# Performance work log

Measured on AMD Instinct MI355X. Metric: run time of the kernel, lower is better.

## Reference

```python
import jax, jax.numpy as jnp
import numpy as np

N_NODES = 100000
IN_CH = 128
HID = 128
OUT_CH = 40
K = 3
N_EDGES = 3200000


def setup_inputs() -> dict:
    key = jax.random.key(0)
    ks = jax.random.split(key, 10)
    x = jax.random.normal(ks[0], (N_NODES, IN_CH), dtype=jnp.float32)
    edge_index = jax.random.randint(ks[1], (2, N_EDGES), 0, N_NODES, dtype=jnp.int64)
    s1 = 1.0 / np.sqrt(IN_CH)
    lin1_w = jax.random.uniform(ks[2], (IN_CH, HID), minval=-s1, maxval=s1, dtype=jnp.float32)
    lin1_b = jax.random.uniform(ks[3], (HID,), minval=-s1, maxval=s1, dtype=jnp.float32)
    s2 = 1.0 / np.sqrt(HID)
    gcn_w = jax.random.uniform(ks[4], (K, HID, HID), minval=-s2, maxval=s2, dtype=jnp.float32)
    gcn_b = jnp.zeros((K, HID), dtype=jnp.float32)
    lin2_w = jax.random.uniform(ks[5], (HID, OUT_CH), minval=-s2, maxval=s2, dtype=jnp.float32)
    lin2_b = jax.random.uniform(ks[6], (OUT_CH,), minval=-s2, maxval=s2, dtype=jnp.float32)
    return {"x": x, "edge_index": edge_index, "lin1_w": lin1_w, "lin1_b": lin1_b,
            "gcn_w": gcn_w, "gcn_b": gcn_b, "lin2_w": lin2_w, "lin2_b": lin2_b}


def _gcn_conv(h, w, b, src, dst, norm, n):
    # PyG GCNConv: transform, then symmetric-normalized aggregation (self-loops
    # already included in src/dst/norm), then bias.
    h = h @ w  # [N, H]
    msg = h[src] * norm[:, None]  # [E+N, H] gathered edge messages
    out = jax.ops.segment_sum(msg, dst, num_segments=n)
    return out + b


def reference(x, edge_index, lin1_w, lin1_b, gcn_w, gcn_b, lin2_w, lin2_b):
    n = x.shape[0]
    src, dst = edge_index[0], edge_index[1]
    # add self-loops (GCNConv default add_self_loops=True)
    loop = jnp.arange(n, dtype=src.dtype)
    src = jnp.concatenate([src, loop])
    dst = jnp.concatenate([dst, loop])
    # symmetric normalization D^{-1/2} (A+I) D^{-1/2}
    deg = jax.ops.segment_sum(jnp.ones(src.shape[0], dtype=x.dtype), dst, num_segments=n)
    dinv = jnp.where(deg > 0, jax.lax.rsqrt(deg), 0.0)
    norm = dinv[src] * dinv[dst]  # [E+N]

    h = jax.nn.relu(x @ lin1_w + lin1_b)  # dropout: eval mode (identity)
    for k in range(K):
        h = jax.nn.relu(_gcn_conv(h, gcn_w[k], gcn_b[k], src, dst, norm, n))
    logits = h @ lin2_w + lin2_b
    return jax.nn.log_softmax(logits, axis=1)
```

## Files before the change

kernel.cpp:

```cpp
#include <hip/hip_runtime.h>
#include <math.h>

#define NN 100000
#define NP 100032
#define HIDC 128
#define OUTC 40
#define NBUCK ((NN + 511) >> 9)
#define PT_TILE 2048
#define BCAP 18368

typedef __attribute__((ext_vector_type(2))) float floatx2;
typedef __attribute__((ext_vector_type(4))) float floatx4;
typedef __attribute__((ext_vector_type(8))) short short8;

__device__ __forceinline__ unsigned pack_bf16x2(float a, float b) {
  unsigned ua = __float_as_uint(a), ub = __float_as_uint(b);
  ua = ua + 0x7fff + ((ua >> 16) & 1);
  ub = ub + 0x7fff + ((ub >> 16) & 1);
  return (ua >> 16) | (ub & 0xffff0000u);
}
__device__ __forceinline__ unsigned short bf16r(float x) {
  unsigned u = __float_as_uint(x);
  u = u + 0x7fff + ((u >> 16) & 1);
  return (unsigned short)(u >> 16);
}


__global__ __launch_bounds__(256) void partition_kernel(
    const int* __restrict__ src, const int* __restrict__ dst,
    int* __restrict__ bcur, unsigned* __restrict__ pairs, int E) {
  __shared__ int hist[256];
  __shared__ int base[256];
  __shared__ int lcur[256];
  int t = threadIdx.x;
  hist[t] = 0; lcur[t] = 0;
  __syncthreads();
  int e0 = blockIdx.x * PT_TILE;
  int ec = E - e0; if (ec > PT_TILE) ec = PT_TILE;
  for (int i = t; i < ec; i += 256)
    atomicAdd(&hist[dst[e0 + i] >> 9], 1);
  __syncthreads();
  if (hist[t] > 0) base[t] = atomicAdd(&bcur[t], hist[t]);
  __syncthreads();
  for (int i = t; i < ec; i += 256) {
    int d = dst[e0 + i], s = src[e0 + i];
    int b = d >> 9;
    int pos = atomicAdd(&lcur[b], 1);
    pairs[base[b] + pos] = ((unsigned)(d & 511) << 17) | (unsigned)s;
  }
}

__global__ __launch_bounds__(1024) void bucket_fill_kernel(
    const unsigned* __restrict__ pairs, const int* __restrict__ bcur,
    float* __restrict__ dinv, int* __restrict__ csr,
    int* __restrict__ sbeg, int* __restrict__ send,
    float* __restrict__ sdinv, int* __restrict__ sdn, int N) {
  int b = blockIdx.x;
  int d0 = b << 9;
  int nd = N - d0; if (nd > 512) nd = 512;
  __shared__ int hist[512];
  __shared__ int cur[512];
  __shared__ int sums[512];
  int t = threadIdx.x;
  if (t < 512) hist[t] = 0;
  __syncthreads();
  int rbeg = b * BCAP, rend = bcur[b];
  for (int i = rbeg + t; i < rend; i += 1024)
    atomicAdd(&hist[pairs[i] >> 17], 1);
  __syncthreads();
  int h = 0;
  if (t < 512) { h = hist[t]; sums[t] = h; }
  __syncthreads();
  for (int off = 1; off < 512; off <<= 1) {
    int u = (t < 512 && t >= off) ? sums[t - off] : 0;
    __syncthreads();
    if (t < 512) sums[t] += u;
    __syncthreads();
  }
  int base = 0; float di = 0.f;
  if (t < 512) {
    base = rbeg + sums[t] - h;
    di = rsqrtf((float)(h + 1));
    if (t < nd) { dinv[d0 + t] = di; cur[t] = base; }
  }
  __syncthreads();

  if (t < 128) hist[t] = 0;
  __syncthreads();
  int c = h < 127 ? h : 127;
  if (t < nd) atomicAdd(&hist[c], 1);
  __syncthreads();
  int dv = (t < 128) ? hist[t] : 0;
  if (t < 128) sums[t] = dv;
  __syncthreads();
  for (int off = 1; off < 128; off <<= 1) {
    int u = (t < 128 && t >= off) ? sums[t - off] : 0;
    __syncthreads();
    if (t < 128) sums[t] += u;
    __syncthreads();
  }
  if (t < 128) hist[128 + t] = sums[t] - dv;
  __syncthreads();
  if (t < nd) {
    int pos = d0 + atomicAdd(&hist[128 + c], 1);
    sbeg[pos] = base; send[pos] = base + h; sdinv[pos] = di; sdn[pos] = d0 + t;
  }
  __syncthreads();

  for (int i = rbeg + t; i < rend; i += 1024) {
    unsigned pk = pairs[i];
    int q = atomicAdd(&cur[pk >> 17], 1);
    csr[q] = pk & 0x1FFFF;
  }
}


__global__ __launch_bounds__(256) void prep_misc_kernel(
    const float* __restrict__ lin1_w, const float* __restrict__ gcn_w,
    const float* __restrict__ lin2_w, int* __restrict__ bcur,
    unsigned short* __restrict__ Wt, unsigned short* __restrict__ W2t) {
  int b = blockIdx.x;
  int t = threadIdx.x;
  if (b == 0) {
    if (t < NBUCK) bcur[t] = t * BCAP;
  } else if (b <= 32) {
    int m = (b - 1) >> 3;
    int chunk = (b - 1) & 7;
    const float* src = (m == 0) ? lin1_w : (gcn_w + (size_t)(m - 1) * 16384);
    unsigned short* dstp = Wt + (size_t)m * 16384;
    int i0 = chunk * 2048;
    for (int i = i0 + t; i < i0 + 2048; i += 256) {
      int n = i >> 7, k = i & 127;
      dstp[(size_t)n * 128 + k] = bf16r(src[(size_t)k * 128 + n]);
    }
  } else {
    int chunk = b - 33;
    int i0 = chunk * 3072;
    for (int i = i0 + t; i < i0 + 3072; i += 256) {
      int n = i >> 7, k = i & 127;
      W2t[i] = (n < OUTC) ? bf16r(lin2_w[(size_t)k * OUTC + n]) : (unsigned short)0;
    }
  }
}


template <int MODE>
__global__ __launch_bounds__(256) void gemm_mfma_kernel(
    const void* __restrict__ Av, const unsigned short* __restrict__ Wt,
    const float* __restrict__ bias, const float* __restrict__ dinv,
    void* __restrict__ Y, int M) {
  int t = threadIdx.x;
  int w = t >> 6;
  int l = t & 63;
  int quad = l >> 4;
  int m16 = l & 15;
  int row0 = blockIdx.x * 64;
  int colbase = w * 32;

  floatx4 acc[4][2];
#pragma unroll
  for (int rt = 0; rt < 4; rt++)
#pragma unroll
    for (int ct = 0; ct < 2; ct++) acc[rt][ct] = (floatx4)0.f;

#pragma unroll
  for (int kc = 0; kc < 4; kc++) {
    int kof = kc * 32 + quad * 8;
    short8 a0 = *(const short8*)(Wt + (size_t)(colbase + m16) * 128 + kof);
    short8 a1 = *(const short8*)(Wt + (size_t)(colbase + 16 + m16) * 128 + kof);
#pragma unroll
    for (int rt = 0; rt < 4; rt++) {
      short8 bfr;
      if (MODE == 2) {
        const float* Af = (const float*)Av + (size_t)(row0 + rt * 16 + m16) * 128 + kof;
        float4 f0 = *(const float4*)Af;
        float4 f1 = *(const float4*)(Af + 4);
        unsigned u0 = pack_bf16x2(f0.x, f0.y);
        unsigned u1 = pack_bf16x2(f0.z, f0.w);
        unsigned u2 = pack_bf16x2(f1.x, f1.y);
        unsigned u3 = pack_bf16x2(f1.z, f1.w);
        bfr[0] = (short)(u0 & 0xFFFF); bfr[1] = (short)(u0 >> 16);
        bfr[2] = (short)(u1 & 0xFFFF); bfr[3] = (short)(u1 >> 16);
        bfr[4] = (short)(u2 & 0xFFFF); bfr[5] = (short)(u2 >> 16);
        bfr[6] = (short)(u3 & 0xFFFF); bfr[7] = (short)(u3 >> 16);
      } else {
        bfr = *(const short8*)((const unsigned short*)Av +
                               (size_t)(row0 + rt * 16 + m16) * 128 + kof);
      }
      acc[rt][0] = __builtin_amdgcn_mfma_f32_16x16x32_bf16(a0, bfr, acc[rt][0], 0, 0, 0);
      acc[rt][1] = __builtin_amdgcn_mfma_f32_16x16x32_bf16(a1, bfr, acc[rt][1], 0, 0, 0);
    }
  }

  if (MODE != 1) {
    unsigned short* Y16 = (unsigned short*)Y;
    float4 bv0 = *(const float4*)(bias + colbase + quad * 4);
    float4 bv1 = *(const float4*)(bias + colbase + 16 + quad * 4);
#pragma unroll
    for (int rt = 0; rt < 4; rt++) {
      int row = row0 + rt * 16 + m16;
      if (row < M) {
        uint2 s0, s1;
        s0.x = pack_bf16x2(fmaxf(acc[rt][0][0] + bv0.x, 0.f),
                           fmaxf(acc[rt][0][1] + bv0.y, 0.f));
        s0.y = pack_bf16x2(fmaxf(acc[rt][0][2] + bv0.z, 0.f),
                           fmaxf(acc[rt][0][3] + bv0.w, 0.f));
        s1.x = pack_bf16x2(fmaxf(acc[rt][1][0] + bv1.x, 0.f),
                           fmaxf(acc[rt][1][1] + bv1.y, 0.f));
        s1.y = pack_bf16x2(fmaxf(acc[rt][1][2] + bv1.z, 0.f),
                           fmaxf(acc[rt][1][3] + bv1.w, 0.f));
        *(uint2*)(Y16 + (size_t)row * 128 + colbase + quad * 4) = s0;
        *(uint2*)(Y16 + (size_t)row * 128 + colbase + 16 + quad * 4) = s1;
      }
    }
  } else {
    unsigned* Y8 = (unsigned*)Y;
#pragma unroll
    for (int rt = 0; rt < 4; rt++) {
      int row = row0 + rt * 16 + m16;
      if (row < M) {
        float dd = dinv[row];
        unsigned u0 = 0, u1 = 0;
        u0 = __builtin_amdgcn_cvt_pk_fp8_f32(acc[rt][0][0] * dd, acc[rt][0][1] * dd, (int)u0, false);
        u0 = __builtin_amdgcn_cvt_pk_fp8_f32(acc[rt][0][2] * dd, acc[rt][0][3] * dd, (int)u0, true);
        u1 = __builtin_amdgcn_cvt_pk_fp8_f32(acc[rt][1][0] * dd, acc[rt][1][1] * dd, (int)u1, false);
        u1 = __builtin_amdgcn_cvt_pk_fp8_f32(acc[rt][1][2] * dd, acc[rt][1][3] * dd, (int)u1, true);
        Y8[(size_t)row * 32 + (colbase >> 2) + quad] = u0;
        Y8[(size_t)row * 32 + ((colbase + 16) >> 2) + quad] = u1;
      }
    }
  }
}


#define ACC8(u)                                                       \
  acc[0] += __builtin_amdgcn_cvt_pk_f32_fp8((int)(u).x, false);       \
  acc[1] += __builtin_amdgcn_cvt_pk_f32_fp8((int)(u).x, true);        \
  acc[2] += __builtin_amdgcn_cvt_pk_f32_fp8((int)(u).y, false);       \
  acc[3] += __builtin_amdgcn_cvt_pk_f32_fp8((int)(u).y, true);        \
  acc[4] += __builtin_amdgcn_cvt_pk_f32_fp8((int)(u).z, false);       \
  acc[5] += __builtin_amdgcn_cvt_pk_f32_fp8((int)(u).z, true);        \
  acc[6] += __builtin_amdgcn_cvt_pk_f32_fp8((int)(u).w, false);       \
  acc[7] += __builtin_amdgcn_cvt_pk_f32_fp8((int)(u).w, true);

__global__ __launch_bounds__(256) void aggregate_fp8_kernel(
    const uint4* __restrict__ Ht8, const int* __restrict__ csr,
    const int* __restrict__ sbeg, const int* __restrict__ send,
    const float* __restrict__ sdinv, const int* __restrict__ sdn,
    const float* __restrict__ bias, uint4* __restrict__ Out, int N) {
  int wid = (blockIdx.x * blockDim.x + threadIdx.x) >> 6;
  int lane = threadIdx.x & 63;
  int g = lane >> 3;
  int c8 = lane & 7;
  int idx = wid * 8 + g;
  if (idx >= N) return;
  int beg = sbeg[idx], end = send[idx];
  int d = sdn[idx];

  floatx2 acc[8];
  {
    uint4 us = Ht8[(size_t)d * 8 + c8];
    acc[0] = __builtin_amdgcn_cvt_pk_f32_fp8((int)us.x, false);
    acc[1] = __builtin_amdgcn_cvt_pk_f32_fp8((int)us.x, true);
    acc[2] = __builtin_amdgcn_cvt_pk_f32_fp8((int)us.y, false);
    acc[3] = __builtin_amdgcn_cvt_pk_f32_fp8((int)us.y, true);
    acc[4] = __builtin_amdgcn_cvt_pk_f32_fp8((int)us.z, false);
    acc[5] = __builtin_amdgcn_cvt_pk_f32_fp8((int)us.z, true);
    acc[6] = __builtin_amdgcn_cvt_pk_f32_fp8((int)us.w, false);
    acc[7] = __builtin_amdgcn_cvt_pk_f32_fp8((int)us.w, true);
  }
  int i = beg;
  int s0, s1, s2, s3, s4, s5, s6, s7;
  if (i + 7 < end) {
    s0 = csr[i];     s1 = csr[i + 1]; s2 = csr[i + 2]; s3 = csr[i + 3];
    s4 = csr[i + 4]; s5 = csr[i + 5]; s6 = csr[i + 6]; s7 = csr[i + 7];
  }
  while (i + 7 < end) {
    uint4 u0 = Ht8[(size_t)s0 * 8 + c8];
    uint4 u1 = Ht8[(size_t)s1 * 8 + c8];
    uint4 u2 = Ht8[(size_t)s2 * 8 + c8];
    uint4 u3 = Ht8[(size_t)s3 * 8 + c8];
    uint4 u4 = Ht8[(size_t)s4 * 8 + c8];
    uint4 u5 = Ht8[(size_t)s5 * 8 + c8];
    uint4 u6 = Ht8[(size_t)s6 * 8 + c8];
    uint4 u7 = Ht8[(size_t)s7 * 8 + c8];
    i += 8;
    if (i + 7 < end) {
      s0 = csr[i];     s1 = csr[i + 1]; s2 = csr[i + 2]; s3 = csr[i + 3];
      s4 = csr[i + 4]; s5 = csr[i + 5]; s6 = csr[i + 6]; s7 = csr[i + 7];
    }
    ACC8(u0) ACC8(u1) ACC8(u2) ACC8(u3) ACC8(u4) ACC8(u5) ACC8(u6) ACC8(u7)
  }
  if (i + 3 < end) {
    int t0 = csr[i], t1 = csr[i + 1], t2 = csr[i + 2], t3 = csr[i + 3];
    uint4 u0 = Ht8[(size_t)t0 * 8 + c8];
    uint4 u1 = Ht8[(size_t)t1 * 8 + c8];
    uint4 u2 = Ht8[(size_t)t2 * 8 + c8];
    uint4 u3 = Ht8[(size_t)t3 * 8 + c8];
    ACC8(u0) ACC8(u1) ACC8(u2) ACC8(u3)
    i += 4;
  }
  for (; i < end; ++i) {
    uint4 u0 = Ht8[(size_t)csr[i] * 8 + c8];
    ACC8(u0)
  }

  float dd = sdinv[idx];
  const float4* b4 = (const float4*)bias;
  float4 bv0 = b4[4 * c8 + 0];
  float4 bv1 = b4[4 * c8 + 1];
  float4 bv2 = b4[4 * c8 + 2];
  float4 bv3 = b4[4 * c8 + 3];
  uint4 o0, o1;
  o0.x = pack_bf16x2(fmaxf(fmaf(dd, acc[0][0], bv0.x), 0.f),
                     fmaxf(fmaf(dd, acc[0][1], bv0.y), 0.f));
  o0.y = pack_bf16x2(fmaxf(fmaf(dd, acc[1][0], bv0.z), 0.f),
                     fmaxf(fmaf(dd, acc[1][1], bv0.w), 0.f));
  o0.z = pack_bf16x2(fmaxf(fmaf(dd, acc[2][0], bv1.x), 0.f),
                     fmaxf(fmaf(dd, acc[2][1], bv1.y), 0.f));
  o0.w = pack_bf16x2(fmaxf(fmaf(dd, acc[3][0], bv1.z), 0.f),
                     fmaxf(fmaf(dd, acc[3][1], bv1.w), 0.f));
  o1.x = pack_bf16x2(fmaxf(fmaf(dd, acc[4][0], bv2.x), 0.f),
                     fmaxf(fmaf(dd, acc[4][1], bv2.y), 0.f));
  o1.y = pack_bf16x2(fmaxf(fmaf(dd, acc[5][0], bv2.z), 0.f),
                     fmaxf(fmaf(dd, acc[5][1], bv2.w), 0.f));
  o1.z = pack_bf16x2(fmaxf(fmaf(dd, acc[6][0], bv3.x), 0.f),
                     fmaxf(fmaf(dd, acc[6][1], bv3.y), 0.f));
  o1.w = pack_bf16x2(fmaxf(fmaf(dd, acc[7][0], bv3.z), 0.f),
                     fmaxf(fmaf(dd, acc[7][1], bv3.w), 0.f));
  Out[(size_t)d * 16 + 2 * c8] = o0;
  Out[(size_t)d * 16 + 2 * c8 + 1] = o1;
}


__global__ __launch_bounds__(256) void head_mfma_kernel(
    const unsigned short* __restrict__ A, const unsigned short* __restrict__ W2t,
    const float* __restrict__ b2, float* __restrict__ Out, int N) {
  __shared__ float lg[64][48];
  __shared__ float bs[48];
  int t = threadIdx.x;
  int w = t >> 6, l = t & 63, quad = l >> 4, m16 = l & 15;
  if (t < 48) bs[t] = (t < OUTC) ? b2[t] : 0.f;
  int row0 = blockIdx.x * 64;

  floatx4 acc[3];
  acc[0] = (floatx4)0.f; acc[1] = (floatx4)0.f; acc[2] = (floatx4)0.f;
  const unsigned short* Aw = A + (size_t)(row0 + w * 16) * 128;
#pragma unroll
  for (int kc = 0; kc < 4; kc++) {
    int kof = kc * 32 + quad * 8;
    short8 a = *(const short8*)(Aw + (size_t)m16 * 128 + kof);
#pragma unroll
    for (int ct = 0; ct < 3; ct++) {
      short8 b = *(const short8*)(W2t + (size_t)(ct * 16 + m16) * 128 + kof);
      acc[ct] = __builtin_amdgcn_mfma_f32_16x16x32_bf16(a, b, acc[ct], 0, 0, 0);
    }
  }
#pragma unroll
  for (int ct = 0; ct < 3; ct++)
#pragma unroll
    for (int j = 0; j < 4; j++)
      lg[w * 16 + quad * 4 + j][ct * 16 + m16] = acc[ct][j];
  __syncthreads();

  int r = t >> 2, sub = t & 3;
  int row = row0 + r;
  float vals[10];
  float mx = -3.4e38f;
#pragma unroll
  for (int j = 0; j < 10; j++) {
    float v = lg[r][sub * 10 + j] + bs[sub * 10 + j];
    vals[j] = v;
    mx = fmaxf(mx, v);
  }
  mx = fmaxf(mx, __shfl_xor(mx, 1, 64));
  mx = fmaxf(mx, __shfl_xor(mx, 2, 64));
  float se = 0.f;
#pragma unroll
  for (int j = 0; j < 10; j++) se += expf(vals[j] - mx);
  se += __shfl_xor(se, 1, 64);
  se += __shfl_xor(se, 2, 64);
  if (row < N) {
    float ls = logf(se);
#pragma unroll
    for (int j = 0; j < 10; j++)
      Out[(size_t)row * OUTC + sub * 10 + j] = vals[j] - mx - ls;
  }
}


extern "C" void kernel_launch(void* const* d_in, const int* in_sizes, int n_in,
                              void* d_out, int out_size, void* d_ws, size_t ws_size,
                              hipStream_t stream) {
  const float* x      = (const float*)d_in[0];
  const int*   edge   = (const int*)d_in[1];
  const float* lin1_w = (const float*)d_in[2];
  const float* lin1_b = (const float*)d_in[3];
  const float* gcn_w  = (const float*)d_in[4];
  const float* gcn_b  = (const float*)d_in[5];
  const float* lin2_w = (const float*)d_in[6];
  const float* lin2_b = (const float*)d_in[7];
  float* out = (float*)d_out;

  const int N = NN;
  const int E = in_sizes[1] / 2;
  const int* src = edge;
  const int* dst = edge + E;

  char* p = (char*)d_ws;
  auto alloc = [&](size_t bytes) { char* q = p; p += (bytes + 255) & ~(size_t)255; return q; };
  unsigned*       hA16    = (unsigned*)alloc((size_t)NP * 128 * 2);
  unsigned*       hB8     = (unsigned*)alloc((size_t)NP * 32 * 4);
  unsigned*       pairs   = (unsigned*)alloc((size_t)NBUCK * BCAP * 4);
  int*            csr     = (int*)alloc((size_t)NBUCK * BCAP * 4);
  float*          dinv    = (float*)alloc((size_t)NP * 4);
  int*            sbeg    = (int*)alloc((size_t)N * 4);
  int*            send    = (int*)alloc((size_t)N * 4);
  float*          sdinv   = (float*)alloc((size_t)N * 4);
  int*            sdn     = (int*)alloc((size_t)N * 4);
  unsigned short* Wt      = (unsigned short*)alloc((size_t)4 * 16384 * 2);
  unsigned short* W2t     = (unsigned short*)alloc((size_t)48 * 128 * 2);
  int*            bcur    = (int*)alloc(256 * 4);

  prep_misc_kernel<<<35, 256, 0, stream>>>(lin1_w, gcn_w, lin2_w, bcur, Wt, W2t);
  partition_kernel<<<(E + PT_TILE - 1) / PT_TILE, 256, 0, stream>>>(src, dst, bcur, pairs, E);
  bucket_fill_kernel<<<NBUCK, 1024, 0, stream>>>(pairs, bcur, dinv, csr,
                                                 sbeg, send, sdinv, sdn, N);

  int gb = NP / 64;
  gemm_mfma_kernel<2><<<gb, 256, 0, stream>>>((const void*)x, Wt,
                                              lin1_b, nullptr, (void*)hA16, N);
  int ablocks = (N / 8 + 3) / 4;
  for (int k = 0; k < 3; k++) {
    gemm_mfma_kernel<1><<<gb, 256, 0, stream>>>((const void*)hA16,
                                                Wt + (size_t)(k + 1) * 16384,
                                                nullptr, dinv, (void*)hB8, N);
    aggregate_fp8_kernel<<<ablocks, 256, 0, stream>>>(
        (const uint4*)hB8, csr, sbeg, send, sdinv, sdn, gcn_b + (size_t)k * 128,
        (uint4*)hA16, N);
  }
  head_mfma_kernel<<<gb, 256, 0, stream>>>((const unsigned short*)hA16, W2t,
                                           lin2_b, out, N);
}
```

Baseline: 509.8 us.

## Stage partitioned edges in LDS for coalesced bucket writes

The edge partition kernel now sorts each tile's edges by destination bucket in shared memory, using a prefix scan and a local buffer, before writing them out. A binary search over bucket starts then maps each output position to its global offset, so consecutive threads write contiguous runs instead of scattering single words. The tile is doubled to 4096 edges with 512 threads, and edges are held in registers to avoid reading them twice. The cost is extra shared memory, a scan with several barriers, a per-element binary search and fewer blocks in flight.

```diff
diff --git a/kernel.cpp b/kernel.cpp
--- a/kernel.cpp
+++ b/kernel.cpp
@@ -6,7 +6,7 @@
 #define HIDC 128
 #define OUTC 40
 #define NBUCK ((NN + 511) >> 9)
-#define PT_TILE 2048
+#define PT_TILE 4096
 #define BCAP 18368
 
 typedef __attribute__((ext_vector_type(2))) float floatx2;
@@ -26,27 +26,68 @@
 }
 
 
-__global__ __launch_bounds__(256) void partition_kernel(
+__global__ __launch_bounds__(512) void partition_kernel(
     const int* __restrict__ src, const int* __restrict__ dst,
     int* __restrict__ bcur, unsigned* __restrict__ pairs, int E) {
   __shared__ int hist[256];
-  __shared__ int base[256];
   __shared__ int lcur[256];
+  __shared__ int startl[256];
+  __shared__ int gofs[256];
+  __shared__ unsigned lbuf[PT_TILE];
   int t = threadIdx.x;
-  hist[t] = 0; lcur[t] = 0;
+  if (t < 256) { hist[t] = 0; lcur[t] = 0; }
   __syncthreads();
   int e0 = blockIdx.x * PT_TILE;
   int ec = E - e0; if (ec > PT_TILE) ec = PT_TILE;
-  for (int i = t; i < ec; i += 256)
-    atomicAdd(&hist[dst[e0 + i] >> 9], 1);
-  __syncthreads();
-  if (hist[t] > 0) base[t] = atomicAdd(&bcur[t], hist[t]);
-  __syncthreads();
-  for (int i = t; i < ec; i += 256) {
-    int d = dst[e0 + i], s = src[e0 + i];
-    int b = d >> 9;
-    int pos = atomicAdd(&lcur[b], 1);
-    pairs[base[b] + pos] = ((unsigned)(d & 511) << 17) | (unsigned)s;
+
+  int dr[8], sr[8];
+#pragma unroll
+  for (int k = 0; k < 8; k++) {
+    int i = t + (k << 9);
+    if (i < ec) {
+      int d = dst[e0 + i];
+      dr[k] = d; sr[k] = src[e0 + i];
+      atomicAdd(&hist[d >> 9], 1);
+    }
+  }
+  __syncthreads();
+
+  int h = (t < 256) ? hist[t] : 0;
+  if (t < 256) startl[t] = h;
+  __syncthreads();
+  for (int off = 1; off < 256; off <<= 1) {
+    int u = (t < 256 && t >= off) ? startl[t - off] : 0;
+    __syncthreads();
+    if (t < 256) startl[t] += u;
+    __syncthreads();
+  }
+  if (t < 256) {
+    int st = startl[t] - h;
+    int gb = (h > 0) ? atomicAdd(&bcur[t], h) : 0;
+    gofs[t] = gb - st;
+    startl[t] = st;
+  }
+  __syncthreads();
+
+#pragma unroll
+  for (int k = 0; k < 8; k++) {
+    int i = t + (k << 9);
+    if (i < ec) {
+      int d = dr[k];
+      int b = d >> 9;
+      int q = atomicAdd(&lcur[b], 1);
+      lbuf[startl[b] + q] = ((unsigned)(d & 511) << 17) | (unsigned)sr[k];
+    }
+  }
+  __syncthreads();
+
+  for (int pos = t; pos < ec; pos += 512) {
+    int lo = 0, hi = 255;
+    while (lo < hi) {
+      int mid = (lo + hi + 1) >> 1;
+      if (startl[mid] <= pos) lo = mid; else hi = mid - 1;
+    }
+    pairs[gofs[lo] + pos] = lbuf[pos];
   }
 }
 
@@ -423,7 +464,7 @@
   int*            bcur    = (int*)alloc(256 * 4);
 
   prep_misc_kernel<<<35, 256, 0, stream>>>(lin1_w, gcn_w, lin2_w, bcur, Wt, W2t);
-  partition_kernel<<<(E + PT_TILE - 1) / PT_TILE, 256, 0, stream>>>(src, dst, bcur, pairs, E);
+  partition_kernel<<<(E + PT_TILE - 1) / PT_TILE, 512, 0, stream>>>(src, dst, bcur, pairs, E);
   bucket_fill_kernel<<<NBUCK, 1024, 0, stream>>>(pairs, bcur, dinv, csr,
                                                  sbeg, send, sdinv, sdn, N);
 
```

Measured after the change: 480.5 us. 1.06x faster.
